# Optimization experiments

Measured on AMD Instinct MI355X. Metric: run time of the kernel, lower is better.

Reference implementation:

```python
import jax, jax.numpy as jnp
import numpy as np

SPATIAL_SHAPES = [(100, 152), (50, 76), (25, 38), (13, 19)]
D_MODEL = 256
N_HEADS = 8
N_LEVELS = 4
N_POINTS = 4
D_FFN = 1024
D_HEAD = D_MODEL // N_HEADS
EPS = 1e-5


def layernorm(x, g, b):
    mu = jnp.mean(x, axis=-1, keepdims=True)
    var = jnp.var(x, axis=-1, keepdims=True)
    return (x - mu) * jax.lax.rsqrt(var + EPS) * g + b


def bilinear_sample(value_l, H, W, locs):
    # value_l: (N, H*W, nH, dH); locs: (N, Lq, nH, P, 2) normalized to [0,1]
    # Matches torch grid_sample(align_corners=False, padding_mode='zeros') with grid=2*loc-1.
    N, Lq = locs.shape[0], locs.shape[1]
    x = locs[..., 0] * W - 0.5  # (N, Lq, nH, P) pixel coords
    y = locs[..., 1] * H - 0.5
    x0 = jnp.floor(x)
    y0 = jnp.floor(y)
    fx = x - x0
    fy = y - y0
    x0 = x0.astype(jnp.int32)
    y0 = y0.astype(jnp.int32)
    out = jnp.zeros((N, Lq, N_POINTS, N_HEADS, D_HEAD), value_l.dtype)
    for dy in (0, 1):
        for dx in (0, 1):
            xi = x0 + dx
            yi = y0 + dy
            w = (fx if dx else 1.0 - fx) * (fy if dy else 1.0 - fy)
            valid = (xi >= 0) & (xi < W) & (yi >= 0) & (yi < H)
            idx = jnp.clip(yi, 0, H - 1) * W + jnp.clip(xi, 0, W - 1)  # (N, Lq, nH, P)
            idx = idx.transpose(0, 1, 3, 2).reshape(N, Lq * N_POINTS, N_HEADS, 1)
            g = jnp.take_along_axis(value_l, idx, axis=1)  # (N, Lq*P, nH, dH)
            g = g.reshape(N, Lq, N_POINTS, N_HEADS, D_HEAD)
            wv = jnp.where(valid, w, 0.0).transpose(0, 1, 3, 2)[..., None]  # (N, Lq, P, nH, 1)
            out = out + g * wv
    return out  # (N, Lq, P, nH, dH)


def msdeform_attn(query, value_in, ref_points,
                  w_value, b_value, w_off, b_off, w_attn, b_attn, w_out, b_out):
    N, Lq, _ = query.shape
    value = (value_in @ w_value + b_value).reshape(N, -1, N_HEADS, D_HEAD)
    off = (query @ w_off + b_off).reshape(N, Lq, N_HEADS, N_LEVELS, N_POINTS, 2)
    attn = (query @ w_attn + b_attn).reshape(N, Lq, N_HEADS, N_LEVELS * N_POINTS)
    attn = jax.nn.softmax(attn, axis=-1).reshape(N, Lq, N_HEADS, N_LEVELS, N_POINTS)
    # offset normalizer is (W, H) per level
    norm = jnp.array([[w, h] for (h, w) in SPATIAL_SHAPES], dtype=query.dtype)  # (L, 2)
    locs = ref_points[:, :, None, :, None, :] + off / norm[None, None, None, :, None, :]
    out = jnp.zeros((N, Lq, N_HEADS, D_HEAD), query.dtype)
    start = 0
    for l, (H, W) in enumerate(SPATIAL_SHAPES):
        v_l = value[:, start:start + H * W]
        s = bilinear_sample(v_l, H, W, locs[:, :, :, l])  # (N, Lq, P, nH, dH)
        out = out + jnp.einsum('nqhp,nqphd->nqhd', attn[:, :, :, l], s)
        start += H * W
    out = out.reshape(N, Lq, D_MODEL)
    return out @ w_out + b_out


def setup_inputs() -> dict:
    key = jax.random.key(0)
    ks = jax.random.split(key, 20)
    B = 2
    Lq = sum(h * w for h, w in SPATIAL_SHAPES)  # 20197
    scale = 0.02
    inp = {
        'src': jax.random.normal(ks[0], (B, Lq, D_MODEL), jnp.float32),
        'pos': jax.random.normal(ks[1], (B, Lq, D_MODEL), jnp.float32),
        'reference_points': jax.random.uniform(ks[2], (B, Lq, N_LEVELS, 2), jnp.float32),
        'spatial_shapes': jnp.array(SPATIAL_SHAPES, dtype=jnp.int32),
        'level_start_index': jnp.array(np.cumsum([0] + [h * w for h, w in SPATIAL_SHAPES[:-1]]), dtype=jnp.int32),
        'w_value': jax.random.normal(ks[3], (D_MODEL, D_MODEL), jnp.float32) * scale,
        'b_value': jnp.zeros((D_MODEL,), jnp.float32),
        'w_off': jax.random.normal(ks[4], (D_MODEL, N_HEADS * N_LEVELS * N_POINTS * 2), jnp.float32) * scale,
        'b_off': jax.random.normal(ks[5], (N_HEADS * N_LEVELS * N_POINTS * 2,), jnp.float32) * scale,
        'w_attn': jax.random.normal(ks[6], (D_MODEL, N_HEADS * N_LEVELS * N_POINTS), jnp.float32) * scale,
        'b_attn': jnp.zeros((N_HEADS * N_LEVELS * N_POINTS,), jnp.float32),
        'w_out': jax.random.normal(ks[7], (D_MODEL, D_MODEL), jnp.float32) * scale,
        'b_out': jnp.zeros((D_MODEL,), jnp.float32),
        'g1': jnp.ones((D_MODEL,), jnp.float32),
        'beta1': jnp.zeros((D_MODEL,), jnp.float32),
        'w1': jax.random.normal(ks[8], (D_MODEL, D_FFN), jnp.float32) * scale,
        'b1': jnp.zeros((D_FFN,), jnp.float32),
        'w2': jax.random.normal(ks[9], (D_FFN, D_MODEL), jnp.float32) * scale,
        'b2': jnp.zeros((D_MODEL,), jnp.float32),
        'g2': jnp.ones((D_MODEL,), jnp.float32),
        'beta2': jnp.zeros((D_MODEL,), jnp.float32),
    }
    return inp


def reference(src, pos, reference_points, spatial_shapes, level_start_index,
              w_value, b_value, w_off, b_off, w_attn, b_attn, w_out, b_out,
              g1, beta1, w1, b1, w2, b2, g2, beta2):
    query = src + pos
    src2 = msdeform_attn(query, src, reference_points,
                         w_value, b_value, w_off, b_off, w_attn, b_attn, w_out, b_out)
    src = layernorm(src + src2, g1, beta1)
    h = jax.nn.relu(src @ w1 + b1)
    src = layernorm(src + h @ w2 + b2, g2, beta2)
    return src
```

## Files before the change

kernel.cpp:

```cpp
#include <hip/hip_runtime.h>

#define LQ   20197
#define MTOT 40394

typedef _Float16 f16;
typedef _Float16 f16x8 __attribute__((ext_vector_type(8)));
typedef _Float16 f16x4 __attribute__((ext_vector_type(4)));
typedef _Float16 f16x2 __attribute__((ext_vector_type(2)));
typedef float    f32x4 __attribute__((ext_vector_type(4)));

#define OFF_WT 0ull
#define OFF_B4 1507328ull
#define OFF_B1 42870784ull
#define OFF_B2 63552512ull
#define OFF_B3 84234240ull
#define OFF_B5 104915968ull
#define OFF_B6 125597696ull

#define WT_V    0
#define WT_OFF  65536
#define WT_ATTN 131072
#define WT_OUT  163840
#define WT_W1   229376
#define WT_W2   491520
#define WT_TOTAL 753664
#define WCONV_TOTAL (WT_TOTAL + 384)

__device__ __forceinline__ void gload_lds16(const f16* g, f16* l) {
    __builtin_amdgcn_global_load_lds(
        (const __attribute__((address_space(1))) unsigned int*)g,
        (__attribute__((address_space(3))) unsigned int*)l,
        16, 0, 0);
}

__global__ __launch_bounds__(256) void k_wconv(
    const float* __restrict__ wv, const float* __restrict__ woff,
    const float* __restrict__ wattn, const float* __restrict__ wout,
    const float* __restrict__ w1, const float* __restrict__ w2,
    const float* __restrict__ boff, const float* __restrict__ battn,
    f16* __restrict__ dst, float* __restrict__ biasoa)
{
    int gid = blockIdx.x * 256 + threadIdx.x;
    if (gid >= WCONV_TOTAL) return;
    if (gid >= WT_TOTAL) {
        int i = gid - WT_TOTAL;
        biasoa[i] = (i < 256) ? boff[i] : battn[i - 256];
        return;
    }
    const float* src; int Kd, Nd, base;
    if      (gid < 65536)  { src = wv;    Kd = 256;  Nd = 256;  base = 0; }
    else if (gid < 131072) { src = woff;  Kd = 256;  Nd = 256;  base = 65536; }
    else if (gid < 163840) { src = wattn; Kd = 256;  Nd = 128;  base = 131072; }
    else if (gid < 229376) { src = wout;  Kd = 256;  Nd = 256;  base = 163840; }
    else if (gid < 491520) { src = w1;    Kd = 256;  Nd = 1024; base = 229376; }
    else                   { src = w2;    Kd = 1024; Nd = 256;  base = 491520; }
    int loc = gid - base;
    int n = loc % Nd, k = loc / Nd;
    dst[base + n * Kd + k] = (f16)src[k * Nd + n];
}

__global__ __launch_bounds__(256) void k_prep(
    const float* __restrict__ src, const float* __restrict__ pos,
    f16* __restrict__ srch, f16* __restrict__ qh, int total4)
{
    int i = blockIdx.x * 256 + threadIdx.x;
    if (i >= total4) return;
    float4 s = ((const float4*)src)[i];
    float4 p = ((const float4*)pos)[i];
    f16x4 hs = { (f16)s.x, (f16)s.y, (f16)s.z, (f16)s.w };
    f16x4 hq = { (f16)(s.x + p.x), (f16)(s.y + p.y), (f16)(s.z + p.z), (f16)(s.w + p.w) };
    ((f16x4*)srch)[i] = hs;
    ((f16x4*)qh)[i]   = hq;
}

template<bool RELU, int OUTM>
__global__ __launch_bounds__(256) void k_gemm128(
    const f16* __restrict__ A, const f16* __restrict__ Bt,
    const float* __restrict__ bias, void* __restrict__ Cout,
    int M, int N, int K)
{
    __shared__ __align__(16) char pool[34816];
    f16* const sm = (f16*)pool;

    const int NBn = N >> 7;
    const int MBn = (M + 127) >> 7;
    const int tiles = MBn * NBn;
    const int q = gridDim.x >> 3;
    const int bid = blockIdx.x;
    const int swz = (bid & 7) * q + (bid >> 3);
    if (swz >= tiles) return;
    const int m0 = (swz / NBn) << 7;
    const int n0 = (swz % NBn) << 7;

    const int t = threadIdx.x, wid = t >> 6, lane = t & 63;

    const int c0 = wid, c1 = wid + 4;
    const int sr = lane >> 2, sk = (lane & 3) * 8;
    const int ra0 = min(m0 + c0 * 16 + sr, M - 1);
    const int ra1 = min(m0 + c1 * 16 + sr, M - 1);
    const f16* pa0 = A + (size_t)ra0 * K + sk;
    const f16* pa1 = A + (size_t)ra1 * K + sk;
    const f16* pb0 = Bt + (size_t)(n0 + c0 * 16 + sr) * K + sk;
    const f16* pb1 = Bt + (size_t)(n0 + c1 * 16 + sr) * K + sk;
    const int lo0 = c0 * 512, lo1 = c1 * 512;

    const int wr = wid >> 1, wc = wid & 1;
    const int fr = lane & 15, kb = (lane >> 4) * 8;

    f32x4 acc[4][4] = {};
    const int NT = K >> 5;

    gload_lds16(pa0, sm + lo0);
    gload_lds16(pa1, sm + lo1);
    gload_lds16(pb0, sm + 4096 + lo0);
    gload_lds16(pb1, sm + 4096 + lo1);
    __syncthreads();

    for (int tt = 0; tt < NT; ++tt) {
        const int cur = (tt & 1) << 13, nxt = cur ^ 8192;
        if (tt + 1 < NT) {
            const int k0 = (tt + 1) << 5;
            gload_lds16(pa0 + k0, sm + nxt + lo0);
            gload_lds16(pa1 + k0, sm + nxt + lo1);
            gload_lds16(pb0 + k0, sm + nxt + 4096 + lo0);
            gload_lds16(pb1 + k0, sm + nxt + 4096 + lo1);
        }
        f16x8 af[4], bf[4];
#pragma unroll
        for (int i = 0; i < 4; ++i)
            af[i] = *(const f16x8*)&sm[cur + (wr * 64 + i * 16 + fr) * 32 + kb];
#pragma unroll
        for (int i = 0; i < 4; ++i)
            bf[i] = *(const f16x8*)&sm[cur + 4096 + (wc * 64 + i * 16 + fr) * 32 + kb];
#pragma unroll
        for (int mi = 0; mi < 4; ++mi)
#pragma unroll
            for (int ni = 0; ni < 4; ++ni)
                acc[mi][ni] = __builtin_amdgcn_mfma_f32_16x16x32_f16(af[mi], bf[ni], acc[mi][ni], 0, 0, 0);
        __syncthreads();
    }

    const int r4 = (lane >> 4) * 4;
#pragma unroll
    for (int ni = 0; ni < 4; ++ni) {
        const int lcol = wc * 64 + ni * 16 + fr;
        const float bv = bias[n0 + lcol];
#pragma unroll
        for (int mi = 0; mi < 4; ++mi) {
#pragma unroll
            for (int j = 0; j < 4; ++j) {
                float v = acc[mi][ni][j] + bv;
                if (RELU) v = fmaxf(v, 0.f);
                sm[(wr * 64 + mi * 16 + r4 + j) * 136 + lcol] = (f16)v;
            }
        }
    }
    __syncthreads();

    if (OUTM == 1) {
        const int rr = t >> 4, cc = (t & 15) * 8;
#pragma unroll
        for (int pass = 0; pass < 8; ++pass) {
            const int r = pass * 16 + rr;
            const int row = m0 + r;
            if (row < M) {
                f16x8 v = *(const f16x8*)&sm[r * 136 + cc];
                *(f16x8*)&((f16*)Cout)[(size_t)row * N + n0 + cc] = v;
            }
        }
    } else {
        const int cbl = t >> 6, rr = (t & 63) >> 2, cc = (t & 3) * 8;
        const size_t cb = (size_t)((n0 >> 5) + cbl);
#pragma unroll
        for (int pass = 0; pass < 8; ++pass) {
            const int r = pass * 16 + rr;
            const int row = m0 + r;
            if (row < M) {
                f16x8 v = *(const f16x8*)&sm[r * 136 + cbl * 32 + cc];
                *(f16x8*)&((f16*)Cout)[(cb * M + row) * 32 + cc] = v;
            }
        }
    }
}

__global__ __launch_bounds__(256) void k_sample(
    const f16* __restrict__ oa, const f16* __restrict__ valueT,
    const float* __restrict__ ref, f16* __restrict__ samp)
{
    __shared__ int4  s_g[2][8][17];
    __shared__ f16x4 s_w[2][8][17];
    const int t = threadIdx.x;
    const int sub = t >> 7;
    const int tok = blockIdx.x * 2 + sub;
    {
        const int h = (t >> 4) & 7, lp = t & 15, l = lp >> 2;
        const size_t row = (size_t)tok * 384;
        float logit = (float)oa[row + 256 + h * 16 + lp];
        float mx = logit;
#pragma unroll
        for (int m = 1; m < 16; m <<= 1) mx = fmaxf(mx, __shfl_xor(mx, m));
        float e = __expf(logit - mx);
        float sum = e;
#pragma unroll
        for (int m = 1; m < 16; m <<= 1) sum += __shfl_xor(sum, m);
        const float aw = e / sum;

        const float fW = (l == 0) ? 152.f : (l == 1) ? 76.f : (l == 2) ? 38.f : 19.f;
        const float fH = (l == 0) ? 100.f : (l == 1) ? 50.f : (l == 2) ? 25.f : 13.f;
        const int   W  = (l == 0) ? 152 : (l == 1) ? 76 : (l == 2) ? 38 : 19;
        const int   H  = (l == 0) ? 100 : (l == 1) ? 50 : (l == 2) ? 25 : 13;
        const int   st = (l == 0) ? 0 : (l == 1) ? 15200 : (l == 2) ? 19000 : 19950;

        const f16x2 ov = *(const f16x2*)&oa[row + h * 32 + lp * 2];
        const float rx = ref[(size_t)tok * 8 + l * 2 + 0];
        const float ry = ref[(size_t)tok * 8 + l * 2 + 1];
        const float x = rx * fW + (float)ov.x - 0.5f;
        const float y = ry * fH + (float)ov.y - 0.5f;
        const float xf = floorf(x), yf = floorf(y);
        const float fx = x - xf, fy = y - yf;
        const int x0 = (int)xf, y0 = (int)yf;

        const bool vx0 = (x0 >= 0) && (x0 < W);
        const bool vx1 = (x0 >= -1) && (x0 < W - 1);
        const bool vy0 = (y0 >= 0) && (y0 < H);
        const bool vy1 = (y0 >= -1) && (y0 < H - 1);
        const int x0c = min(max(x0, 0), W - 1), x1c = min(max(x0 + 1, 0), W - 1);
        const int y0c = min(max(y0, 0), H - 1), y1c = min(max(y0 + 1, 0), H - 1);

        const int n = (tok >= LQ) ? 1 : 0;
        const int i00 = n * LQ + st + y0c * W + x0c;
        const int dxs = x1c - x0c, dys = (y1c - y0c) * W;
        s_g[sub][h][lp] = make_int4(i00, i00 + dxs, i00 + dys, i00 + dys + dxs);

        const float w00 = (vx0 && vy0) ? (1.f - fx) * (1.f - fy) * aw : 0.f;
        const float w01 = (vx1 && vy0) ? fx * (1.f - fy) * aw : 0.f;
        const float w10 = (vx0 && vy1) ? (1.f - fx) * fy * aw : 0.f;
        const float w11 = (vx1 && vy1) ? fx * fy * aw : 0.f;
        f16x4 wv = { (f16)w00, (f16)w01, (f16)w10, (f16)w11 };
        s_w[sub][h][lp] = wv;
    }
    __syncthreads();

    const int h = (t >> 4) & 7, ln = t & 15;
    const unsigned int tb4 = ((unsigned int)h * (MTOT * 16u) + ln) * 4u;
    const char* vbase = (const char*)valueT;
    float ax = 0.f, ay = 0.f;
#pragma unroll 4
    for (int p = 0; p < 16; ++p) {
        const int4  g  = s_g[sub][h][p];
        const f16x4 w4 = s_w[sub][h][p];
        const f16x2 v00 = *(const f16x2*)(vbase + (tb4 + ((unsigned int)g.x << 6)));
        const f16x2 v01 = *(const f16x2*)(vbase + (tb4 + ((unsigned int)g.y << 6)));
        const f16x2 v10 = *(const f16x2*)(vbase + (tb4 + ((unsigned int)g.z << 6)));
        const f16x2 v11 = *(const f16x2*)(vbase + (tb4 + ((unsigned int)g.w << 6)));
        const f16x2 wl = { w4.x, w4.y }, wh = { w4.z, w4.w };
        const f16x2 A1 = __builtin_shufflevector(v00, v01, 0, 2);
        const f16x2 B1 = __builtin_shufflevector(v00, v01, 1, 3);
        const f16x2 A2 = __builtin_shufflevector(v10, v11, 0, 2);
        const f16x2 B2 = __builtin_shufflevector(v10, v11, 1, 3);
        ax = __builtin_amdgcn_fdot2(A1, wl, ax, false);
        ax = __builtin_amdgcn_fdot2(A2, wh, ax, false);
        ay = __builtin_amdgcn_fdot2(B1, wl, ay, false);
        ay = __builtin_amdgcn_fdot2(B2, wh, ay, false);
    }
    f16x2 o = { (f16)ax, (f16)ay };
    *(f16x2*)&samp[(size_t)tok * 256 + h * 32 + ln * 2] = o;
}

__global__ __launch_bounds__(256) void k_ln1(
    const float* __restrict__ xa, const f16* __restrict__ xb,
    const float* __restrict__ g, const float* __restrict__ be,
    f16* __restrict__ yh, int M)
{
    const int row = blockIdx.x * 4 + (threadIdx.x >> 6);
    const int lane = threadIdx.x & 63;
    if (row >= M) return;
    const size_t o = (size_t)row * 256 + lane * 4;
    float4 a = *(const float4*)(xa + o);
    f16x4  b = *(const f16x4*)(xb + o);
    float x0 = a.x + (float)b.x, x1 = a.y + (float)b.y;
    float x2 = a.z + (float)b.z, x3 = a.w + (float)b.w;
    float s  = x0 + x1 + x2 + x3;
    float ss = x0*x0 + x1*x1 + x2*x2 + x3*x3;
#pragma unroll
    for (int m = 1; m < 64; m <<= 1) { s += __shfl_xor(s, m); ss += __shfl_xor(ss, m); }
    const float mean = s * (1.f / 256.f);
    const float var  = ss * (1.f / 256.f) - mean * mean;
    const float rstd = rsqrtf(var + 1e-5f);
    float4 gv = *(const float4*)(g + lane * 4);
    float4 bv = *(const float4*)(be + lane * 4);
    f16x4 hv = { (f16)((x0 - mean) * rstd * gv.x + bv.x),
                 (f16)((x1 - mean) * rstd * gv.y + bv.y),
                 (f16)((x2 - mean) * rstd * gv.z + bv.z),
                 (f16)((x3 - mean) * rstd * gv.w + bv.w) };
    *(f16x4*)(yh + o) = hv;
}

__global__ __launch_bounds__(256) void k_ln2(
    const f16* __restrict__ xa, const f16* __restrict__ xb,
    const float* __restrict__ g, const float* __restrict__ be,
    float* __restrict__ yf, int M)
{
    const int row = blockIdx.x * 4 + (threadIdx.x >> 6);
    const int lane = threadIdx.x & 63;
    if (row >= M) return;
    const size_t o = (size_t)row * 256 + lane * 4;
    f16x4 a = *(const f16x4*)(xa + o);
    f16x4 b = *(const f16x4*)(xb + o);
    float x0 = (float)a.x + (float)b.x, x1 = (float)a.y + (float)b.y;
    float x2 = (float)a.z + (float)b.z, x3 = (float)a.w + (float)b.w;
    float s  = x0 + x1 + x2 + x3;
    float ss = x0*x0 + x1*x1 + x2*x2 + x3*x3;
#pragma unroll
    for (int m = 1; m < 64; m <<= 1) { s += __shfl_xor(s, m); ss += __shfl_xor(ss, m); }
    const float mean = s * (1.f / 256.f);
    const float var  = ss * (1.f / 256.f) - mean * mean;
    const float rstd = rsqrtf(var + 1e-5f);
    float4 gv = *(const float4*)(g + lane * 4);
    float4 bv = *(const float4*)(be + lane * 4);
    float4 yo = { (x0 - mean) * rstd * gv.x + bv.x,
                  (x1 - mean) * rstd * gv.y + bv.y,
                  (x2 - mean) * rstd * gv.z + bv.z,
                  (x3 - mean) * rstd * gv.w + bv.w };
    *(float4*)(yf + o) = yo;
}

extern "C" void kernel_launch(void* const* d_in, const int* in_sizes, int n_in,
                              void* d_out, int out_size, void* d_ws, size_t ws_size,
                              hipStream_t stream) {
    const float* src   = (const float*)d_in[0];
    const float* pos   = (const float*)d_in[1];
    const float* ref   = (const float*)d_in[2];
    const float* w_value = (const float*)d_in[5];
    const float* b_value = (const float*)d_in[6];
    const float* w_off   = (const float*)d_in[7];
    const float* b_off   = (const float*)d_in[8];
    const float* w_attn  = (const float*)d_in[9];
    const float* b_attn  = (const float*)d_in[10];
    const float* w_out   = (const float*)d_in[11];
    const float* b_out   = (const float*)d_in[12];
    const float* g1    = (const float*)d_in[13];
    const float* beta1 = (const float*)d_in[14];
    const float* w1    = (const float*)d_in[15];
    const float* b1    = (const float*)d_in[16];
    const float* w2    = (const float*)d_in[17];
    const float* b2    = (const float*)d_in[18];
    const float* g2    = (const float*)d_in[19];
    const float* beta2 = (const float*)d_in[20];

    char* ws = (char*)d_ws;
    f16*   wT      = (f16*)(ws + OFF_WT);
    f16*   oa      = (f16*)(ws + OFF_B4);
    f16*   y2h     = (f16*)(ws + OFF_B4);
    f16*   srch    = (f16*)(ws + OFF_B1);
    f16*   samph   = (f16*)(ws + OFF_B1);
    f16*   qh      = (f16*)(ws + OFF_B2);
    f16*   x1h     = (f16*)(ws + OFF_B2);
    f16*   valueT  = (f16*)(ws + OFF_B3);
    f16*   hh      = (f16*)(ws + OFF_B3);
    float* biasoa  = (float*)(ws + OFF_B5);
    f16*   src2h   = (f16*)(ws + OFF_B6);
    float* outp    = (float*)d_out;

    const int M = MTOT;
    const int MB = (M + 127) / 128;
    auto grid8 = [&](int nb) { return ((MB * nb) + 7) & ~7; };

    k_wconv<<<(WCONV_TOTAL + 255) / 256, 256, 0, stream>>>(
        w_value, w_off, w_attn, w_out, w1, w2, b_off, b_attn, wT, biasoa);
    k_prep<<<(M * 64 + 255) / 256, 256, 0, stream>>>(src, pos, srch, qh, M * 64);

    k_gemm128<false, 2><<<grid8(2), 256, 0, stream>>>(srch, wT + WT_V, b_value, valueT, M, 256, 256);
    k_gemm128<false, 1><<<grid8(3), 256, 0, stream>>>(qh, wT + WT_OFF, biasoa, oa, M, 384, 256);
    k_sample<<<dim3(MTOT / 2), 256, 0, stream>>>(oa, valueT, ref, samph);
    k_gemm128<false, 1><<<grid8(2), 256, 0, stream>>>(samph, wT + WT_OUT, b_out, src2h, M, 256, 256);
    k_ln1<<<(M + 3) / 4, 256, 0, stream>>>(src, src2h, g1, beta1, x1h, M);
    k_gemm128<true, 1><<<grid8(8), 256, 0, stream>>>(x1h, wT + WT_W1, b1, hh, M, 1024, 256);
    k_gemm128<false, 1><<<grid8(2), 256, 0, stream>>>(hh, wT + WT_W2, b2, y2h, M, 256, 1024);
    k_ln2<<<(M + 3) / 4, 256, 0, stream>>>(x1h, y2h, g2, beta2, outp, M);

    (void)in_sizes; (void)n_in; (void)out_size; (void)ws_size;
}
```

Before: 221.2 us.

## Widen deformable sampling gathers to 16-byte loads, 8 tokens per block

```diff
diff --git a/kernel.cpp b/kernel.cpp
--- a/kernel.cpp
+++ b/kernel.cpp
@@ -187,84 +187,98 @@
     const f16* __restrict__ oa, const f16* __restrict__ valueT,
     const float* __restrict__ ref, f16* __restrict__ samp)
 {
-    __shared__ int4  s_g[2][8][17];
-    __shared__ f16x4 s_w[2][8][17];
+    __shared__ uint4 s_g[8][8][17];
+    __shared__ f16x8 s_w[8][8][17];
     const int t = threadIdx.x;
-    const int sub = t >> 7;
-    const int tok = blockIdx.x * 2 + sub;
-    {
-        const int h = (t >> 4) & 7, lp = t & 15, l = lp >> 2;
-        const size_t row = (size_t)tok * 384;
-        float logit = (float)oa[row + 256 + h * 16 + lp];
-        float mx = logit;
-#pragma unroll
-        for (int m = 1; m < 16; m <<= 1) mx = fmaxf(mx, __shfl_xor(mx, m));
-        float e = __expf(logit - mx);
-        float sum = e;
-#pragma unroll
-        for (int m = 1; m < 16; m <<= 1) sum += __shfl_xor(sum, m);
-        const float aw = e / sum;
-
-        const float fW = (l == 0) ? 152.f : (l == 1) ? 76.f : (l == 2) ? 38.f : 19.f;
-        const float fH = (l == 0) ? 100.f : (l == 1) ? 50.f : (l == 2) ? 25.f : 13.f;
-        const int   W  = (l == 0) ? 152 : (l == 1) ? 76 : (l == 2) ? 38 : 19;
-        const int   H  = (l == 0) ? 100 : (l == 1) ? 50 : (l == 2) ? 25 : 13;
-        const int   st = (l == 0) ? 0 : (l == 1) ? 15200 : (l == 2) ? 19000 : 19950;
-
-        const f16x2 ov = *(const f16x2*)&oa[row + h * 32 + lp * 2];
-        const float rx = ref[(size_t)tok * 8 + l * 2 + 0];
-        const float ry = ref[(size_t)tok * 8 + l * 2 + 1];
-        const float x = rx * fW + (float)ov.x - 0.5f;
-        const float y = ry * fH + (float)ov.y - 0.5f;
-        const float xf = floorf(x), yf = floorf(y);
-        const float fx = x - xf, fy = y - yf;
-        const int x0 = (int)xf, y0 = (int)yf;
-
-        const bool vx0 = (x0 >= 0) && (x0 < W);
-        const bool vx1 = (x0 >= -1) && (x0 < W - 1);
-        const bool vy0 = (y0 >= 0) && (y0 < H);
-        const bool vy1 = (y0 >= -1) && (y0 < H - 1);
-        const int x0c = min(max(x0, 0), W - 1), x1c = min(max(x0 + 1, 0), W - 1);
-        const int y0c = min(max(y0, 0), H - 1), y1c = min(max(y0 + 1, 0), H - 1);
-
-        const int n = (tok >= LQ) ? 1 : 0;
-        const int i00 = n * LQ + st + y0c * W + x0c;
-        const int dxs = x1c - x0c, dys = (y1c - y0c) * W;
-        s_g[sub][h][lp] = make_int4(i00, i00 + dxs, i00 + dys, i00 + dys + dxs);
-
-        const float w00 = (vx0 && vy0) ? (1.f - fx) * (1.f - fy) * aw : 0.f;
-        const float w01 = (vx1 && vy0) ? fx * (1.f - fy) * aw : 0.f;
-        const float w10 = (vx0 && vy1) ? (1.f - fx) * fy * aw : 0.f;
-        const float w11 = (vx1 && vy1) ? fx * fy * aw : 0.f;
-        f16x4 wv = { (f16)w00, (f16)w01, (f16)w10, (f16)w11 };
-        s_w[sub][h][lp] = wv;
+    const int tok0 = blockIdx.x * 8;
+
+#pragma unroll
+    for (int it = 0; it < 4; ++it) {
+        const int gid = it * 256 + t;
+        const int tl = gid >> 7, h = (gid >> 4) & 7, lp = gid & 15, l = lp >> 2;
+        const int tok = tok0 + tl;
+        if (tok < MTOT) {
+            const size_t row = (size_t)tok * 384;
+            float logit = (float)oa[row + 256 + h * 16 + lp];
+            float mx = logit;
+#pragma unroll
+            for (int m = 1; m < 16; m <<= 1) mx = fmaxf(mx, __shfl_xor(mx, m));
+            float e = __expf(logit - mx);
+            float sum = e;
+#pragma unroll
+            for (int m = 1; m < 16; m <<= 1) sum += __shfl_xor(sum, m);
+            const float aw = e / sum;
+
+            const float fW = (l == 0) ? 152.f : (l == 1) ? 76.f : (l == 2) ? 38.f : 19.f;
+            const float fH = (l == 0) ? 100.f : (l == 1) ? 50.f : (l == 2) ? 25.f : 13.f;
+            const int   W  = (l == 0) ? 152 : (l == 1) ? 76 : (l == 2) ? 38 : 19;
+            const int   H  = (l == 0) ? 100 : (l == 1) ? 50 : (l == 2) ? 25 : 13;
+            const int   st = (l == 0) ? 0 : (l == 1) ? 15200 : (l == 2) ? 19000 : 19950;
+
+            const f16x2 ov = *(const f16x2*)&oa[row + h * 32 + lp * 2];
+            const float2 rxy = *(const float2*)&ref[(size_t)tok * 8 + l * 2];
+            const float x = rxy.x * fW + (float)ov.x - 0.5f;
+            const float y = rxy.y * fH + (float)ov.y - 0.5f;
+            const float xf = floorf(x), yf = floorf(y);
+            const float fx = x - xf, fy = y - yf;
+            const int x0 = (int)xf, y0 = (int)yf;
+
+            const bool vx0 = (x0 >= 0) && (x0 < W);
+            const bool vx1 = (x0 >= -1) && (x0 < W - 1);
+            const bool vy0 = (y0 >= 0) && (y0 < H);
+            const bool vy1 = (y0 >= -1) && (y0 < H - 1);
+            const int x0c = min(max(x0, 0), W - 1), x1c = min(max(x0 + 1, 0), W - 1);
+            const int y0c = min(max(y0, 0), H - 1), y1c = min(max(y0 + 1, 0), H - 1);
+
+            const int n = (tok >= LQ) ? 1 : 0;
+            const unsigned int b00 = ((unsigned int)(n * LQ + st + y0c * W + x0c) << 6)
+                                   + (unsigned int)h * (MTOT * 64u);
+            const unsigned int dx6 = (unsigned int)(x1c - x0c) << 6;
+            const unsigned int dy6 = (unsigned int)((y1c - y0c) * W) << 6;
+            s_g[tl][h][lp] = make_uint4(b00, b00 + dx6, b00 + dy6, b00 + dy6 + dx6);
+
+            const f16 w00 = (f16)((vx0 && vy0) ? (1.f - fx) * (1.f - fy) * aw : 0.f);
+            const f16 w01 = (f16)((vx1 && vy0) ? fx * (1.f - fy) * aw : 0.f);
+            const f16 w10 = (f16)((vx0 && vy1) ? (1.f - fx) * fy * aw : 0.f);
+            const f16 w11 = (f16)((vx1 && vy1) ? fx * fy * aw : 0.f);
+            f16x8 wv = { w00, w00, w01, w01, w10, w10, w11, w11 };
+            s_w[tl][h][lp] = wv;
+        }
     }
     __syncthreads();
 
-    const int h = (t >> 4) & 7, ln = t & 15;
-    const unsigned int tb4 = ((unsigned int)h * (MTOT * 16u) + ln) * 4u;
+    const int tl = t >> 5, h = (t >> 2) & 7, l4 = t & 3;
+    const int tok = tok0 + tl;
+    if (tok >= MTOT) return;
+    const unsigned int lb = (unsigned int)l4 * 16u;
     const char* vbase = (const char*)valueT;
-    float ax = 0.f, ay = 0.f;
+
+    f16x2 a0 = {}, a1 = {}, a2 = {}, a3 = {};
 #pragma unroll 4
     for (int p = 0; p < 16; ++p) {
-        const int4  g  = s_g[sub][h][p];
-        const f16x4 w4 = s_w[sub][h][p];
-        const f16x2 v00 = *(const f16x2*)(vbase + (tb4 + ((unsigned int)g.x << 6)));
-        const f16x2 v01 = *(const f16x2*)(vbase + (tb4 + ((unsigned int)g.y << 6)));
-        const f16x2 v10 = *(const f16x2*)(vbase + (tb4 + ((unsigned int)g.z << 6)));
-        const f16x2 v11 = *(const f16x2*)(vbase + (tb4 + ((unsigned int)g.w << 6)));
-        const f16x2 wl = { w4.x, w4.y }, wh = { w4.z, w4.w };
-        const f16x2 A1 = __builtin_shufflevector(v00, v01, 0, 2);
-        const f16x2 B1 = __builtin_shufflevector(v00, v01, 1, 3);
-        const f16x2 A2 = __builtin_shufflevector(v10, v11, 0, 2);
-        const f16x2 B2 = __builtin_shufflevector(v10, v11, 1, 3);
-        ax = __builtin_amdgcn_fdot2(A1, wl, ax, false);
-        ax = __builtin_amdgcn_fdot2(A2, wh, ax, false);
-        ay = __builtin_amdgcn_fdot2(B1, wl, ay, false);
-        ay = __builtin_amdgcn_fdot2(B2, wh, ay, false);
-    }
-    f16x2 o = { (f16)ax, (f16)ay };
-    *(f16x2*)&samp[(size_t)tok * 256 + h * 32 + ln * 2] = o;
+        const uint4 g  = s_g[tl][h][p];
+        const f16x8 wv = s_w[tl][h][p];
+        const f16x8 v00 = *(const f16x8*)(vbase + (g.x + lb));
+        const f16x8 v01 = *(const f16x8*)(vbase + (g.y + lb));
+        const f16x8 v10 = *(const f16x8*)(vbase + (g.z + lb));
+        const f16x8 v11 = *(const f16x8*)(vbase + (g.w + lb));
+        const f16x2 w00 = { wv[0], wv[1] }, w01 = { wv[2], wv[3] };
+        const f16x2 w10 = { wv[4], wv[5] }, w11 = { wv[6], wv[7] };
+        const f16x2* p00 = (const f16x2*)&v00;
+        const f16x2* p01 = (const f16x2*)&v01;
+        const f16x2* p10 = (const f16x2*)&v10;
+        const f16x2* p11 = (const f16x2*)&v11;
+        a0 = a0 + p00[0] * w00; a1 = a1 + p00[1] * w00;
+        a2 = a2 + p00[2] * w00; a3 = a3 + p00[3] * w00;
+        a0 = a0 + p01[0] * w01; a1 = a1 + p01[1] * w01;
+        a2 = a2 + p01[2] * w01; a3 = a3 + p01[3] * w01;
+        a0 = a0 + p10[0] * w10; a1 = a1 + p10[1] * w10;
+        a2 = a2 + p10[2] * w10; a3 = a3 + p10[3] * w10;
+        a0 = a0 + p11[0] * w11; a1 = a1 + p11[1] * w11;
+        a2 = a2 + p11[2] * w11; a3 = a3 + p11[3] * w11;
+    }
+    f16x8 o = { a0.x, a0.y, a1.x, a1.y, a2.x, a2.y, a3.x, a3.y };
+    *(f16x8*)&samp[(size_t)tok * 256 + h * 32 + l4 * 8] = o;
 }
 
 __global__ __launch_bounds__(256) void k_ln1(
@@ -372,7 +386,7 @@
 
     k_gemm128<false, 2><<<grid8(2), 256, 0, stream>>>(srch, wT + WT_V, b_value, valueT, M, 256, 256);
     k_gemm128<false, 1><<<grid8(3), 256, 0, stream>>>(qh, wT + WT_OFF, biasoa, oa, M, 384, 256);
-    k_sample<<<dim3(MTOT / 2), 256, 0, stream>>>(oa, valueT, ref, samph);
+    k_sample<<<dim3((MTOT + 7) / 8), 256, 0, stream>>>(oa, valueT, ref, samph);
     k_gemm128<false, 1><<<grid8(2), 256, 0, stream>>>(samph, wT + WT_OUT, b_out, src2h, M, 256, 256);
     k_ln1<<<(M + 3) / 4, 256, 0, stream>>>(src, src2h, g1, beta1, x1h, M);
     k_gemm128<true, 1><<<grid8(8), 256, 0, stream>>>(x1h, wT + WT_W1, b1, hh, M, 1024, 256);
```

Measured after the change: 227.8 us. 1.03x slower.
